# Performance work log

Measured on AMD Instinct MI355X. Metric: run time of the kernel, lower is better.

The kernel has to match this reference:

```python
import jax, jax.numpy as jnp
import numpy as np

EPS = 1e-13

def masked_softmax(scores, mask):
    # scores: [B, L1, L2], mask: [B, L2] binary float
    # ESIM-style: softmax(scores * mask) * mask, renormalized.
    m = mask[:, None, :]                      # [B, 1, L2]
    r = jax.nn.softmax(scores * m, axis=-1) * m
    return r / (r.sum(axis=-1, keepdims=True) + EPS)

def weighted_sum(attn, tensor, mask):
    # attn: [B, L1, L2], tensor: [B, L2, D], mask: [B, L1]
    return jnp.matmul(attn, tensor) * mask[:, :, None]

def setup_inputs() -> dict:
    key = jax.random.key(0)
    k1, k2, k3, k4 = jax.random.split(key, 4)
    B, Lp, Lh, D = 64, 512, 512, 600
    encoded_premise = jax.random.normal(k1, (B, Lp, D), dtype=jnp.float32)
    encoded_hypothesis = jax.random.normal(k2, (B, Lh, D), dtype=jnp.float32)
    # binary padding masks (1 = valid token)
    premise_mask = (jax.random.uniform(k3, (B, Lp)) > 0.15).astype(jnp.float32)
    hypothesis_mask = (jax.random.uniform(k4, (B, Lh)) > 0.15).astype(jnp.float32)
    return {"encoded_premise": encoded_premise, "premise_mask": premise_mask,
            "encoded_hypothesis": encoded_hypothesis, "hypothesis_mask": hypothesis_mask}

def reference(encoded_premise, premise_mask, encoded_hypothesis, hypothesis_mask):
    # shared cross-attention score matrix [B, Lp, Lh]
    attn = jnp.einsum('bpd,bhd->bph', encoded_premise, encoded_hypothesis)
    a_p = masked_softmax(attn, hypothesis_mask)                    # [B, Lp, Lh]
    a_h = masked_softmax(attn.transpose(0, 2, 1), premise_mask)    # [B, Lh, Lp]
    weighted_premise = weighted_sum(a_p, encoded_hypothesis, premise_mask)      # [B, Lp, D]
    weighted_hypothesis = weighted_sum(a_h, encoded_premise, hypothesis_mask)   # [B, Lh, D]
    return (weighted_premise, weighted_hypothesis)
```

## Files before the change

kernel.cpp:

```cpp
#include <hip/hip_runtime.h>
#include <hip/hip_bf16.h>

#define DEVB 64
#define LSEQ 512
#define DDIM 600

typedef short short8 __attribute__((ext_vector_type(8)));
typedef float f32x4 __attribute__((ext_vector_type(4)));
typedef _Float16 f16x8 __attribute__((ext_vector_type(8)));
typedef _Float16 f16x4 __attribute__((ext_vector_type(4)));

constexpr int LDP = 40;

__device__ __forceinline__ unsigned short f2bf(float x) {
    union { float f; unsigned u; } v; v.f = x;
    unsigned r = v.u + 0x7fffu + ((v.u >> 16) & 1u);
    return (unsigned short)(r >> 16);
}
__device__ __forceinline__ unsigned pk16(float a, float b) {
    union { _Float16 h[2]; unsigned u; } p;
    p.h[0] = (_Float16)a; p.h[1] = (_Float16)b;
    return p.u;
}
__device__ __forceinline__ f32x4 mfma16(short8 a, short8 b, f32x4 c) {
    return __builtin_amdgcn_mfma_f32_16x16x32_bf16(a, b, c, 0, 0, 0);
}
__device__ __forceinline__ f32x4 mfma16h(f16x8 a, f16x8 b, f32x4 c) {
    return __builtin_amdgcn_mfma_f32_16x16x32_f16(a, b, c, 0, 0, 0);
}

__global__ __launch_bounds__(256) void transcvt3(
    const float* __restrict__ P, const float* __restrict__ H,
    _Float16* __restrict__ pT, _Float16* __restrict__ hT)
{
    int blk = blockIdx.x;
    const float* X; _Float16* XT;
    const int half = DEVB * 40;
    if (blk < half) { X = P; XT = pT; }
    else { blk -= half; X = H; XT = hT; }

    int b   = blk / 40;
    int rem = blk % 40;
    int r0  = (rem / 5) << 6;
    int d0  = (rem % 5) << 7;
    const float* Xb = X + (size_t)b * LSEQ * DDIM;

    __shared__ unsigned T32[2][64 * 33];
    const int t  = threadIdx.x;
    const int rp = t >> 3;
    const int dc = (t & 7) << 3;

#pragma unroll
    for (int ht_ = 0; ht_ < 2; ++ht_) {
        int dd = d0 + (ht_ << 6) + dc;
        if (dd < DDIM) {
            const float* s0 = Xb + (size_t)(r0 + 2 * rp) * DDIM + dd;
            const float* s1 = s0 + DDIM;
            float4 a0 = *(const float4*)s0, a1 = *(const float4*)(s0 + 4);
            float4 b0 = *(const float4*)s1, b1 = *(const float4*)(s1 + 4);
            float xa[8] = {a0.x, a0.y, a0.z, a0.w, a1.x, a1.y, a1.z, a1.w};
            float xb[8] = {b0.x, b0.y, b0.z, b0.w, b1.x, b1.y, b1.z, b1.w};
#pragma unroll
            for (int j = 0; j < 8; ++j)
                T32[ht_][(dc + j) * 33 + rp] = pk16(xa[j], xb[j]);
        }
    }
    __syncthreads();

    const int dl = t >> 2;
    const int q  = t & 3;
#pragma unroll
    for (int ht_ = 0; ht_ < 2; ++ht_) {
        int d = d0 + (ht_ << 6) + dl;
        if (d < DDIM) {
            unsigned buf[8];
#pragma unroll
            for (int i = 0; i < 8; ++i)
                buf[i] = T32[ht_][dl * 33 + q * 8 + i];
            unsigned* dst = (unsigned*)(XT + ((size_t)b * DDIM + d) * LSEQ + r0) + q * 8;
            *(uint4*)(dst)     = *(uint4*)&buf[0];
            *(uint4*)(dst + 4) = *(uint4*)&buf[4];
        }
    }
}

__global__ __launch_bounds__(256) void attn_gemm(
    const float* __restrict__ P, const float* __restrict__ H,
    float* __restrict__ attn)
{
    const int bid = blockIdx.x;
    const int swz = (bid & 7) * 128 + (bid >> 3);
    const int b  = swz >> 4;
    const int pt = ((swz >> 2) & 3) << 7;
    const int ht = (swz & 3) << 7;
    const float* Pb = P + ((size_t)b * LSEQ + pt) * DDIM;
    const float* Hb = H + ((size_t)b * LSEQ + ht) * DDIM;
    float* Ab = attn + (size_t)b * LSEQ * LSEQ;

    __shared__ _Float16 Ah[2][128 * 32], Al[2][128 * 32], Bh[2][128 * 32];

    const int t    = threadIdx.x;
    const int lane = t & 63;
    const int wave = t >> 6;
    const int wm = (wave >> 1) << 6;
    const int wn = (wave & 1) << 6;
    const int fr = lane & 15;
    const int fq = lane >> 4;
    const int srow = t >> 2;
    const int sc8  = (t & 3) << 3;

    const int wchunk = (t & 3) ^ ((srow >> 1) & 3);
    const int woff   = srow * 32 + (wchunk << 3);
    const int rcoff  = ((fq ^ ((fr >> 1) & 3)) << 3);

    float4 pf[8];
    const float4 fz = {0.f, 0.f, 0.f, 0.f};
    auto issue = [&](int k0) {
        bool ok = (k0 + sc8) < DDIM;
#pragma unroll
        for (int r = 0; r < 2; ++r) {
            size_t base = (size_t)(srow + (r << 6)) * DDIM + k0 + sc8;
            if (ok) {
                pf[r * 4 + 0] = *(const float4*)(Pb + base);
                pf[r * 4 + 1] = *(const float4*)(Pb + base + 4);
                pf[r * 4 + 2] = *(const float4*)(Hb + base);
                pf[r * 4 + 3] = *(const float4*)(Hb + base + 4);
            } else {
                pf[r * 4 + 0] = fz; pf[r * 4 + 1] = fz;
                pf[r * 4 + 2] = fz; pf[r * 4 + 3] = fz;
            }
        }
    };
    auto wr = [&](int buf) {
#pragma unroll
        for (int r = 0; r < 2; ++r) {
            float4 a0 = pf[r * 4 + 0], a1 = pf[r * 4 + 1];
            float4 h0 = pf[r * 4 + 2], h1 = pf[r * 4 + 3];
            float af[8] = {a0.x, a0.y, a0.z, a0.w, a1.x, a1.y, a1.z, a1.w};
            float hf[8] = {h0.x, h0.y, h0.z, h0.w, h1.x, h1.y, h1.z, h1.w};
            f16x8 hi, lo, bh;
#pragma unroll
            for (int j = 0; j < 8; ++j) {
                hi[j] = (_Float16)af[j];
                lo[j] = (_Float16)(af[j] - (float)hi[j]);
                bh[j] = (_Float16)hf[j];
            }
            int off = woff + (r << 11);
            *(f16x8*)&Ah[buf][off] = hi;
            *(f16x8*)&Al[buf][off] = lo;
            *(f16x8*)&Bh[buf][off] = bh;
        }
    };

    issue(0);
    wr(0);
    issue(32);
    __syncthreads();

    f32x4 acc[4][4];
#pragma unroll
    for (int i = 0; i < 4; ++i)
#pragma unroll
        for (int j = 0; j < 4; ++j) acc[i][j] = (f32x4){0.f, 0.f, 0.f, 0.f};

    constexpr int NK = 19;
    int cur = 0;
    for (int it = 0; it < NK; ++it) {
        f16x8 ah[4], al[4], bh[4];
#pragma unroll
        for (int i = 0; i < 4; ++i) {
            int ra = (wm + (i << 4) + fr) * 32 + rcoff;
            int rb = (wn + (i << 4) + fr) * 32 + rcoff;
            ah[i] = *(const f16x8*)&Ah[cur][ra];
            al[i] = *(const f16x8*)&Al[cur][ra];
            bh[i] = *(const f16x8*)&Bh[cur][rb];
        }
        if (it + 1 < NK) {
            wr(cur ^ 1);
            if (it + 2 < NK) issue((it + 2) << 5);
        }
#pragma unroll
        for (int mi = 0; mi < 4; ++mi)
#pragma unroll
            for (int ni = 0; ni < 4; ++ni) {
                f32x4 c = acc[mi][ni];
                c = mfma16h(ah[mi], bh[ni], c);
                c = mfma16h(al[mi], bh[ni], c);
                acc[mi][ni] = c;
            }
        __syncthreads();
        cur ^= 1;
    }

#pragma unroll
    for (int mi = 0; mi < 4; ++mi)
#pragma unroll
        for (int ni = 0; ni < 4; ++ni)
#pragma unroll
            for (int j = 0; j < 4; ++j) {
                int p = pt + wm + (mi << 4) + (fq << 2) + j;
                int h = ht + wn + (ni << 4) + fr;
                Ab[(size_t)p * LSEQ + h] = acc[mi][ni][j];
            }
}

__global__ __launch_bounds__(256) void stats_w1(
    const float* __restrict__ attn, const float* __restrict__ hmask,
    const float* __restrict__ pmask,
    float* __restrict__ M1, float* __restrict__ R1,
    _Float16* __restrict__ W1,
    float* __restrict__ Mp, float* __restrict__ Tp, float* __restrict__ Sp)
{
    int b      = blockIdx.x >> 3;
    int stripe = blockIdx.x & 7;
    int lane   = threadIdx.x & 63;
    int wave   = threadIdx.x >> 6;
    const float* hm = hmask + (b << 9);
    const float* pm = pmask + (b << 9);

    float4 m0 = *(const float4*)(hm + (lane << 3));
    float4 m1 = *(const float4*)(hm + (lane << 3) + 4);
    float mk[8] = {m0.x, m0.y, m0.z, m0.w, m1.x, m1.y, m1.z, m1.w};

    float cM[8], cT[8], cS[8];
#pragma unroll
    for (int j = 0; j < 8; ++j) { cM[j] = -1e30f; cT[j] = 0.f; cS[j] = 0.f; }

    for (int i = 0; i < 16; ++i) {
        int row   = (stripe << 6) + (wave << 4) + i;
        int rowid = (b << 9) + row;
        const float* rp = attn + (size_t)rowid * LSEQ + (lane << 3);
        float4 s0 = *(const float4*)rp;
        float4 s1 = *(const float4*)(rp + 4);
        float s[8] = {s0.x, s0.y, s0.z, s0.w, s1.x, s1.y, s1.z, s1.w};

        float v[8];
#pragma unroll
        for (int j = 0; j < 8; ++j) v[j] = s[j] * mk[j];
        float mx = -1e30f;
#pragma unroll
        for (int j = 0; j < 8; ++j) mx = fmaxf(mx, v[j]);
#pragma unroll
        for (int off = 32; off; off >>= 1) mx = fmaxf(mx, __shfl_xor(mx, off));

        float e[8], T = 0.f, S = 0.f;
#pragma unroll
        for (int j = 0; j < 8; ++j) { e[j] = __expf(v[j] - mx); T += mk[j] * e[j]; S += e[j]; }
#pragma unroll
        for (int off = 32; off; off >>= 1) { T += __shfl_xor(T, off); S += __shfl_xor(S, off); }
        float R = 1.f / (T + 1e-13f * S);

        if (W1) {
            union { f16x8 v8; _Float16 h[8]; } wv;
#pragma unroll
            for (int j = 0; j < 8; ++j) wv.h[j] = (_Float16)(mk[j] * e[j] * R);
            *(f16x8*)(W1 + (size_t)rowid * LSEQ + (lane << 3)) = wv.v8;
        }
        if (lane == 0) { M1[rowid] = mx; R1[rowid] = R; }

        float pmv = pm[row];
#pragma unroll
        for (int j = 0; j < 8; ++j) {
            float v2 = s[j] * pmv;
            float nm = fmaxf(cM[j], v2);
            float sc = __expf(cM[j] - nm);
            float e2 = __expf(v2 - nm);
            cT[j] = cT[j] * sc + pmv * e2;
            cS[j] = cS[j] * sc + e2;
            cM[j] = nm;
        }
    }

    __shared__ float LM[4][512], LT[4][512], LS[4][512];
#pragma unroll
    for (int j = 0; j < 8; ++j) {
        int c = (lane << 3) + j;
        LM[wave][c] = cM[j]; LT[wave][c] = cT[j]; LS[wave][c] = cS[j];
    }
    __syncthreads();

    size_t base = (size_t)((b << 3) + stripe) * 512;
    for (int cc = threadIdx.x; cc < 512; cc += 256) {
        float gm = fmaxf(fmaxf(LM[0][cc], LM[1][cc]), fmaxf(LM[2][cc], LM[3][cc]));
        float gT = 0.f, gS = 0.f;
#pragma unroll
        for (int w = 0; w < 4; ++w) {
            float sc = __expf(LM[w][cc] - gm);
            gT += LT[w][cc] * sc;
            gS += LS[w][cc] * sc;
        }
        Mp[base + cc] = gm; Tp[base + cc] = gT; Sp[base + cc] = gS;
    }
}

__global__ __launch_bounds__(256) void col_merge(
    const float* __restrict__ Mp, const float* __restrict__ Tp,
    const float* __restrict__ Sp, float* __restrict__ M2, float* __restrict__ R2)
{
    int b = blockIdx.x >> 1;
    int c = ((blockIdx.x & 1) << 8) + threadIdx.x;
    float gm = -1e30f, gT = 0.f, gS = 0.f;
#pragma unroll
    for (int st = 0; st < 8; ++st) {
        size_t idx = (size_t)((b << 3) + st) * 512 + c;
        float m = Mp[idx], tt = Tp[idx], ss = Sp[idx];
        float nm  = fmaxf(gm, m);
        float sc1 = __expf(gm - nm), sc2 = __expf(m - nm);
        gT = gT * sc1 + tt * sc2;
        gS = gS * sc1 + ss * sc2;
        gm = nm;
    }
    M2[(b << 9) + c] = gm;
    R2[(b << 9) + c] = 1.f / (gT + 1e-13f * gS);
}

__global__ __launch_bounds__(256) void w2gen3(
    const float* __restrict__ attn, const float* __restrict__ pmask,
    const float* __restrict__ Mp, const float* __restrict__ Tp,
    const float* __restrict__ Sp, _Float16* __restrict__ W2)
{
    int blk = blockIdx.x;
    int b  = blk >> 5;
    int p0 = ((blk >> 2) & 7) << 6;
    int h0 = (blk & 3) << 7;
    const float* Ab = attn + (size_t)b * LSEQ * LSEQ;
    const float* pm = pmask + (b << 9);

    __shared__ float sM[128], sR[128];
    __shared__ unsigned T32[128 * 33];
    const int t = threadIdx.x;
    if (t < 128) {
        float gm = -1e30f, gT = 0.f, gS = 0.f;
#pragma unroll
        for (int st = 0; st < 8; ++st) {
            size_t idx = (size_t)((b << 3) + st) * 512 + h0 + t;
            float m = Mp[idx], tt = Tp[idx], ss = Sp[idx];
            float nm  = fmaxf(gm, m);
            float sc1 = __expf(gm - nm), sc2 = __expf(m - nm);
            gT = gT * sc1 + tt * sc2;
            gS = gS * sc1 + ss * sc2;
            gm = nm;
        }
        sM[t] = gm;
        sR[t] = 1.f / (gT + 1e-13f * gS);
    }
    __syncthreads();

#pragma unroll
    for (int it = 0; it < 4; ++it) {
        int g  = t + (it << 8);
        int pp = g >> 5;
        int hc = (g & 31) << 2;
        const float* s0 = Ab + (size_t)(p0 + 2 * pp) * LSEQ + h0 + hc;
        float4 xa = *(const float4*)s0;
        float4 xb = *(const float4*)(s0 + LSEQ);
        float pa = pm[p0 + 2 * pp];
        float pb = pm[p0 + 2 * pp + 1];
        float a[4] = {xa.x, xa.y, xa.z, xa.w};
        float bb[4] = {xb.x, xb.y, xb.z, xb.w};
#pragma unroll
        for (int j = 0; j < 4; ++j) {
            float wa = (pa != 0.f) ? __expf(a[j]  - sM[hc + j]) * sR[hc + j] : 0.f;
            float wb = (pb != 0.f) ? __expf(bb[j] - sM[hc + j]) * sR[hc + j] : 0.f;
            T32[(hc + j) * 33 + pp] = pk16(wa, wb);
        }
    }
    __syncthreads();

    const int hl = t >> 1;
    const int q  = t & 1;
    unsigned buf[16];
#pragma unroll
    for (int i = 0; i < 16; ++i)
        buf[i] = T32[hl * 33 + q * 16 + i];
    unsigned* dst = (unsigned*)(W2 + ((size_t)(b << 9) + h0 + hl) * LSEQ + p0) + q * 16;
#pragma unroll
    for (int i = 0; i < 4; ++i)
        *(uint4*)(dst + 4 * i) = *(uint4*)&buf[4 * i];
}

__global__ __launch_bounds__(256) void gemm_fp16(
    const _Float16* __restrict__ W, const _Float16* __restrict__ BT,
    const float* __restrict__ mask_m, float* __restrict__ out)
{
    const int bid = blockIdx.x;
    const int swz = (bid & 7) * 160 + (bid >> 3);
    const int b   = swz / 20;
    const int rem = swz % 20;
    const int m0  = (rem / 5) << 7;
    const int n0  = (rem % 5) << 7;
    const _Float16* Wb = W  + (size_t)b * LSEQ * LSEQ;
    const _Float16* Bb = BT + (size_t)b * DDIM * LSEQ;

    __shared__ _Float16 Wl[2][128 * 32];
    __shared__ _Float16 Bl[2][128 * 32];

    const int t    = threadIdx.x;
    const int lane = t & 63;
    const int wave = t >> 6;
    const int wm = (wave >> 1) << 6;
    const int wn = (wave & 1) << 6;
    const int fr = lane & 15;
    const int fq = lane >> 4;
    const int srow = t >> 2;
    const int sc8  = (t & 3) << 3;

    const int wchunk = (t & 3) ^ ((srow >> 1) & 3);
    const int woff   = srow * 32 + (wchunk << 3);
    const int rcoff  = ((fq ^ ((fr >> 1) & 3)) << 3);

    f16x8 pw[2], pb[2];
    const f16x8 zz = {0, 0, 0, 0, 0, 0, 0, 0};
    auto issue = [&](int k0) {
#pragma unroll
        for (int r = 0; r < 2; ++r) {
            int row = srow + (r << 6);
            pw[r] = *(const f16x8*)(Wb + (size_t)(m0 + row) * LSEQ + k0 + sc8);
            int nrow = n0 + row;
            pb[r] = (nrow < DDIM) ? *(const f16x8*)(Bb + (size_t)nrow * LSEQ + k0 + sc8) : zz;
        }
    };
    auto wr = [&](int buf) {
#pragma unroll
        for (int r = 0; r < 2; ++r) {
            int off = woff + (r << 11);
            *(f16x8*)&Wl[buf][off] = pw[r];
            *(f16x8*)&Bl[buf][off] = pb[r];
        }
    };

    issue(0);
    wr(0);
    issue(32);
    __syncthreads();

    f32x4 acc[4][4];
#pragma unroll
    for (int i = 0; i < 4; ++i)
#pragma unroll
        for (int j = 0; j < 4; ++j) acc[i][j] = (f32x4){0.f, 0.f, 0.f, 0.f};

    constexpr int NK = 16;
    int cur = 0;
    for (int it = 0; it < NK; ++it) {
        f16x8 af[4], bfr[4];
#pragma unroll
        for (int i = 0; i < 4; ++i) {
            af[i]  = *(const f16x8*)&Wl[cur][(wm + (i << 4) + fr) * 32 + rcoff];
            bfr[i] = *(const f16x8*)&Bl[cur][(wn + (i << 4) + fr) * 32 + rcoff];
        }
        if (it + 1 < NK) {
            wr(cur ^ 1);
            if (it + 2 < NK) issue((it + 2) << 5);
        }
#pragma unroll
        for (int mi = 0; mi < 4; ++mi)
#pragma unroll
            for (int ni = 0; ni < 4; ++ni)
                acc[mi][ni] = mfma16h(af[mi], bfr[ni], acc[mi][ni]);
        __syncthreads();
        cur ^= 1;
    }

    const float* mmb = mask_m + (b << 9) + m0;
#pragma unroll
    for (int mi = 0; mi < 4; ++mi)
#pragma unroll
        for (int j = 0; j < 4; ++j) {
            int row = wm + (mi << 4) + (fq << 2) + j;
            float mm = mmb[row];
#pragma unroll
            for (int ni = 0; ni < 4; ++ni) {
                int d = n0 + wn + (ni << 4) + fr;
                if (d < DDIM)
                    out[((size_t)(b << 9) + m0 + row) * DDIM + d] = mm * acc[mi][ni][j];
            }
        }
}

template <int TRANSA>
__global__ __launch_bounds__(256) void wsum(
    const float* __restrict__ attn, const float* __restrict__ Bsrc,
    const float* __restrict__ mask_k, const float* __restrict__ mask_m,
    const float* __restrict__ Mst, const float* __restrict__ Rst,
    float* __restrict__ out)
{
    const int blk = blockIdx.x;
    const int b   = blk / 20;
    const int rem = blk % 20;
    const int m0  = (rem / 5) << 7;
    const int n0  = (rem % 5) << 7;

    const float* Ab  = attn + (size_t)b * LSEQ * LSEQ;
    const float* Bb  = Bsrc + (size_t)b * LSEQ * DDIM;
    const float* mkb = mask_k + (b << 9);

    __shared__ unsigned short Wl[128 * LDP];
    __shared__ unsigned short Bl[128 * LDP];
    __shared__ float Ml[128], Rl[128], Mm[128];

    const int t    = threadIdx.x;
    const int lane = t & 63;
    const int wave = t >> 6;
    const int wm = (wave >> 1) << 6;
    const int wn = (wave & 1) << 6;
    const int fr = lane & 15;
    const int fq = lane >> 4;

    if (t < 128) {
        Ml[t] = Mst[(b << 9) + m0 + t];
        Rl[t] = Rst[(b << 9) + m0 + t];
        Mm[t] = mask_m[(b << 9) + m0 + t];
    }
    __syncthreads();

    f32x4 acc[4][4];
#pragma unroll
    for (int i = 0; i < 4; ++i)
#pragma unroll
        for (int j = 0; j < 4; ++j) acc[i][j] = (f32x4){0.f, 0.f, 0.f, 0.f};

    for (int k0 = 0; k0 < LSEQ; k0 += 32) {
        if constexpr (TRANSA == 0) {
#pragma unroll
            for (int r = 0; r < 4; ++r) {
                int idx = t + (r << 8);
                int row = idx >> 3;
                int c4  = (idx & 7) << 2;
                float4 x  = *(const float4*)(Ab + (size_t)(m0 + row) * LSEQ + k0 + c4);
                float4 km = *(const float4*)(mkb + k0 + c4);
                float Mv = Ml[row], Rv = Rl[row];
                ushort4 w;
                w.x = (km.x != 0.f) ? f2bf(__expf(x.x - Mv) * Rv) : (unsigned short)0;
                w.y = (km.y != 0.f) ? f2bf(__expf(x.y - Mv) * Rv) : (unsigned short)0;
                w.z = (km.z != 0.f) ? f2bf(__expf(x.z - Mv) * Rv) : (unsigned short)0;
                w.w = (km.w != 0.f) ? f2bf(__expf(x.w - Mv) * Rv) : (unsigned short)0;
                *(ushort4*)&Wl[row * LDP + c4] = w;
            }
        } else {
#pragma unroll
            for (int r = 0; r < 4; ++r) {
                int mh = t & 127;
                int pq = (t >> 7) + (r << 1);
                float Mv = Ml[mh], Rv = Rl[mh];
                ushort4 w;
#pragma unroll
                for (int j = 0; j < 4; ++j) {
                    int k = k0 + (pq << 2) + j;
                    float x  = Ab[(size_t)k * LSEQ + m0 + mh];
                    float km = mkb[k];
                    ((unsigned short*)&w)[j] =
                        (km != 0.f) ? f2bf(__expf(x - Mv) * Rv) : (unsigned short)0;
                }
                *(ushort4*)&Wl[mh * LDP + (pq << 2)] = w;
            }
        }
#pragma unroll
        for (int r = 0; r < 4; ++r) {
            int d  = t & 127;
            int kq = (t >> 7) + (r << 1);
            bool valid = (n0 + d) < DDIM;
            ushort4 v;
#pragma unroll
            for (int j = 0; j < 4; ++j) {
                int k = k0 + (kq << 2) + j;
                float x = valid ? Bb[(size_t)k * DDIM + n0 + d] : 0.f;
                ((unsigned short*)&v)[j] = f2bf(x);
            }
            *(ushort4*)&Bl[d * LDP + (kq << 2)] = v;
        }
        __syncthreads();

        short8 af[4], bfr[4];
#pragma unroll
        for (int i = 0; i < 4; ++i) {
            af[i]  = *(const short8*)&Wl[(wm + (i << 4) + fr) * LDP + (fq << 3)];
            bfr[i] = *(const short8*)&Bl[(wn + (i << 4) + fr) * LDP + (fq << 3)];
        }
#pragma unroll
        for (int mi = 0; mi < 4; ++mi)
#pragma unroll
            for (int ni = 0; ni < 4; ++ni)
                acc[mi][ni] = mfma16(af[mi], bfr[ni], acc[mi][ni]);
        __syncthreads();
    }

#pragma unroll
    for (int mi = 0; mi < 4; ++mi)
#pragma unroll
        for (int j = 0; j < 4; ++j) {
            int row = wm + (mi << 4) + (fq << 2) + j;
            float mm = Mm[row];
#pragma unroll
            for (int ni = 0; ni < 4; ++ni) {
                int d = n0 + wn + (ni << 4) + fr;
                if (d < DDIM)
                    out[((size_t)(b << 9) + m0 + row) * DDIM + d] = mm * acc[mi][ni][j];
            }
        }
}

extern "C" void kernel_launch(void* const* d_in, const int* in_sizes, int n_in,
                              void* d_out, int out_size, void* d_ws, size_t ws_size,
                              hipStream_t stream)
{
    const float* P  = (const float*)d_in[0];
    const float* pm = (const float*)d_in[1];
    const float* H  = (const float*)d_in[2];
    const float* hm = (const float*)d_in[3];
    float* out = (float*)d_out;
    char* o  = (char*)d_out;
    char* ws = (char*)d_ws;

    const size_t E = (size_t)DEVB * LSEQ * DDIM;

    _Float16* hT = (_Float16*)(o + 78643200);
    _Float16* W1 = (_Float16*)(o + 117964800);

    const size_t fast_need = 143654912;

    if (ws_size >= fast_need) {
        float*     attn = (float*)ws;
        _Float16*  pT   = (_Float16*)(ws + 67108864);
        _Float16*  W2   = (_Float16*)(ws + 67108864 + 39321600);
        float*     Mp   = (float*)(ws + 139984896);
        float*     Tp   = Mp + (size_t)DEVB * 8 * 512;
        float*     Sp   = Tp + (size_t)DEVB * 8 * 512;
        float*     M1   = Sp + (size_t)DEVB * 8 * 512;
        float*     R1   = M1 + DEVB * LSEQ;

        transcvt3<<<DEVB * 80, 256, 0, stream>>>(P, H, pT, hT);
        attn_gemm<<<DEVB * 16, 256, 0, stream>>>(P, H, attn);
        stats_w1<<<DEVB * 8, 256, 0, stream>>>(attn, hm, pm, M1, R1, W1, Mp, Tp, Sp);
        w2gen3<<<DEVB * 32, 256, 0, stream>>>(attn, pm, Mp, Tp, Sp, W2);
        gemm_fp16<<<DEVB * 20, 256, 0, stream>>>(W1, hT, pm, out);
        gemm_fp16<<<DEVB * 20, 256, 0, stream>>>(W2, pT, hm, out + E);
    } else {
        float* attn = (float*)ws;
        float* Mp   = (float*)(ws + 67108864);
        float* Tp   = Mp + (size_t)DEVB * 8 * 512;
        float* Sp   = Tp + (size_t)DEVB * 8 * 512;
        float* M1   = Sp + (size_t)DEVB * 8 * 512;
        float* R1   = M1 + DEVB * LSEQ;
        float* M2   = R1 + DEVB * LSEQ;
        float* R2   = M2 + DEVB * LSEQ;

        attn_gemm<<<DEVB * 16, 256, 0, stream>>>(P, H, attn);
        stats_w1<<<DEVB * 8, 256, 0, stream>>>(attn, hm, pm, M1, R1, nullptr, Mp, Tp, Sp);
        col_merge<<<DEVB * 2, 256, 0, stream>>>(Mp, Tp, Sp, M2, R2);
        wsum<0><<<DEVB * 20, 256, 0, stream>>>(attn, H, hm, pm, M1, R1, out);
        wsum<1><<<DEVB * 20, 256, 0, stream>>>(attn, P, pm, hm, M2, R2, out + E);
    }
}
```

Before: 321.4 us.

## Fuse transpose-convert into weighted-sum GEMM and merge both GEMMs into one launch

Result: no change. 315.1 us (-1.9%).

```diff
diff --git a/kernel.cpp b/kernel.cpp
--- a/kernel.cpp
+++ b/kernel.cpp
@@ -27,61 +27,6 @@
 }
 __device__ __forceinline__ f32x4 mfma16h(f16x8 a, f16x8 b, f32x4 c) {
     return __builtin_amdgcn_mfma_f32_16x16x32_f16(a, b, c, 0, 0, 0);
-}
-
-__global__ __launch_bounds__(256) void transcvt3(
-    const float* __restrict__ P, const float* __restrict__ H,
-    _Float16* __restrict__ pT, _Float16* __restrict__ hT)
-{
-    int blk = blockIdx.x;
-    const float* X; _Float16* XT;
-    const int half = DEVB * 40;
-    if (blk < half) { X = P; XT = pT; }
-    else { blk -= half; X = H; XT = hT; }
-
-    int b   = blk / 40;
-    int rem = blk % 40;
-    int r0  = (rem / 5) << 6;
-    int d0  = (rem % 5) << 7;
-    const float* Xb = X + (size_t)b * LSEQ * DDIM;
-
-    __shared__ unsigned T32[2][64 * 33];
-    const int t  = threadIdx.x;
-    const int rp = t >> 3;
-    const int dc = (t & 7) << 3;
-
-#pragma unroll
-    for (int ht_ = 0; ht_ < 2; ++ht_) {
-        int dd = d0 + (ht_ << 6) + dc;
-        if (dd < DDIM) {
-            const float* s0 = Xb + (size_t)(r0 + 2 * rp) * DDIM + dd;
-            const float* s1 = s0 + DDIM;
-            float4 a0 = *(const float4*)s0, a1 = *(const float4*)(s0 + 4);
-            float4 b0 = *(const float4*)s1, b1 = *(const float4*)(s1 + 4);
-            float xa[8] = {a0.x, a0.y, a0.z, a0.w, a1.x, a1.y, a1.z, a1.w};
-            float xb[8] = {b0.x, b0.y, b0.z, b0.w, b1.x, b1.y, b1.z, b1.w};
-#pragma unroll
-            for (int j = 0; j < 8; ++j)
-                T32[ht_][(dc + j) * 33 + rp] = pk16(xa[j], xb[j]);
-        }
-    }
-    __syncthreads();
-
-    const int dl = t >> 2;
-    const int q  = t & 3;
-#pragma unroll
-    for (int ht_ = 0; ht_ < 2; ++ht_) {
-        int d = d0 + (ht_ << 6) + dl;
-        if (d < DDIM) {
-            unsigned buf[8];
-#pragma unroll
-            for (int i = 0; i < 8; ++i)
-                buf[i] = T32[ht_][dl * 33 + q * 8 + i];
-            unsigned* dst = (unsigned*)(XT + ((size_t)b * DDIM + d) * LSEQ + r0) + q * 8;
-            *(uint4*)(dst)     = *(uint4*)&buf[0];
-            *(uint4*)(dst + 4) = *(uint4*)&buf[4];
-        }
-    }
 }
 
 __global__ __launch_bounds__(256) void attn_gemm(
@@ -379,21 +324,31 @@
         *(uint4*)(dst + 4 * i) = *(uint4*)&buf[4 * i];
 }
 
-__global__ __launch_bounds__(256) void gemm_fp16(
-    const _Float16* __restrict__ W, const _Float16* __restrict__ BT,
-    const float* __restrict__ mask_m, float* __restrict__ out)
+__global__ __launch_bounds__(256) void gemm_dual(
+    const _Float16* __restrict__ W1, const _Float16* __restrict__ W2,
+    const float* __restrict__ P, const float* __restrict__ H,
+    const float* __restrict__ pmask, const float* __restrict__ hmask,
+    float* __restrict__ out)
 {
-    const int bid = blockIdx.x;
+    int bid = blockIdx.x;
+    const _Float16* W; const float* Bsrc; const float* maskm; float* o;
+    if (bid < DEVB * 20) {
+        W = W1; Bsrc = H; maskm = pmask; o = out;
+    } else {
+        bid -= DEVB * 20;
+        W = W2; Bsrc = P; maskm = hmask;
+        o = out + (size_t)DEVB * LSEQ * DDIM;
+    }
     const int swz = (bid & 7) * 160 + (bid >> 3);
     const int b   = swz / 20;
     const int rem = swz % 20;
     const int m0  = (rem / 5) << 7;
     const int n0  = (rem % 5) << 7;
-    const _Float16* Wb = W  + (size_t)b * LSEQ * LSEQ;
-    const _Float16* Bb = BT + (size_t)b * DDIM * LSEQ;
+    const _Float16* Wb = W + (size_t)b * LSEQ * LSEQ;
+    const float*    Bb = Bsrc + (size_t)b * LSEQ * DDIM;
 
     __shared__ _Float16 Wl[2][128 * 32];
-    __shared__ _Float16 Bl[2][128 * 32];
+    __shared__ unsigned Bl[2][128 * 20];
 
     const int t    = threadIdx.x;
     const int lane = t & 63;
@@ -402,30 +357,47 @@
     const int wn = (wave & 1) << 6;
     const int fr = lane & 15;
     const int fq = lane >> 4;
+
     const int srow = t >> 2;
     const int sc8  = (t & 3) << 3;
-
     const int wchunk = (t & 3) ^ ((srow >> 1) & 3);
-    const int woff   = srow * 32 + (wchunk << 3);
+    const int woffA  = srow * 32 + (wchunk << 3);
     const int rcoff  = ((fq ^ ((fr >> 1) & 3)) << 3);
 
-    f16x8 pw[2], pb[2];
-    const f16x8 zz = {0, 0, 0, 0, 0, 0, 0, 0};
+    const int kp = t >> 4;
+    const int dg = t & 15;
+    const int dcol = n0 + (dg << 3);
+    const bool bok = dcol < DDIM;
+
+    f16x8 pw[2];
+    float4 pbv[4];
+    const float4 fz = {0.f, 0.f, 0.f, 0.f};
     auto issue = [&](int k0) {
-#pragma unroll
-        for (int r = 0; r < 2; ++r) {
-            int row = srow + (r << 6);
-            pw[r] = *(const f16x8*)(Wb + (size_t)(m0 + row) * LSEQ + k0 + sc8);
-            int nrow = n0 + row;
-            pb[r] = (nrow < DDIM) ? *(const f16x8*)(Bb + (size_t)nrow * LSEQ + k0 + sc8) : zz;
-        }
+        pw[0] = *(const f16x8*)(Wb + (size_t)(m0 + srow) * LSEQ + k0 + sc8);
+        pw[1] = *(const f16x8*)(Wb + (size_t)(m0 + srow + 64) * LSEQ + k0 + sc8);
+        if (bok) {
+            const float* r0 = Bb + (size_t)(k0 + 2 * kp) * DDIM + dcol;
+            const float* r1 = r0 + DDIM;
+            pbv[0] = *(const float4*)r0;
+            pbv[1] = *(const float4*)(r0 + 4);
+            pbv[2] = *(const float4*)r1;
+            pbv[3] = *(const float4*)(r1 + 4);
+        } else { pbv[0] = fz; pbv[1] = fz; pbv[2] = fz; pbv[3] = fz; }
     };
     auto wr = [&](int buf) {
-#pragma unroll
-        for (int r = 0; r < 2; ++r) {
-            int off = woff + (r << 11);
-            *(f16x8*)&Wl[buf][off] = pw[r];
-            *(f16x8*)&Bl[buf][off] = pb[r];
+        *(f16x8*)&Wl[buf][woffA]             = pw[0];
+        *(f16x8*)&Wl[buf][woffA + (64 * 32)] = pw[1];
+        float a[8] = {pbv[0].x, pbv[0].y, pbv[0].z, pbv[0].w,
+                      pbv[1].x, pbv[1].y, pbv[1].z, pbv[1].w};
+        float c[8] = {pbv[2].x, pbv[2].y, pbv[2].z, pbv[2].w,
+                      pbv[3].x, pbv[3].y, pbv[3].z, pbv[3].w};
+        unsigned w[8];
+#pragma unroll
+        for (int j = 0; j < 8; ++j) w[j] = pk16(a[j], c[j]);
+#pragma unroll
+        for (int jo = 0; jo < 8; ++jo) {
+            int jj = (jo + dg) & 7;
+            Bl[buf][((dg << 3) + jj) * 20 + kp] = w[jj];
         }
     };
 
@@ -446,8 +418,10 @@
         f16x8 af[4], bfr[4];
 #pragma unroll
         for (int i = 0; i < 4; ++i) {
-            af[i]  = *(const f16x8*)&Wl[cur][(wm + (i << 4) + fr) * 32 + rcoff];
-            bfr[i] = *(const f16x8*)&Bl[cur][(wn + (i << 4) + fr) * 32 + rcoff];
+            af[i] = *(const f16x8*)&Wl[cur][(wm + (i << 4) + fr) * 32 + rcoff];
+            union { uint4 u; f16x8 h; } bu;
+            bu.u = *(const uint4*)&Bl[cur][(wn + (i << 4) + fr) * 20 + (fq << 2)];
+            bfr[i] = bu.h;
         }
         if (it + 1 < NK) {
             wr(cur ^ 1);
@@ -462,7 +436,7 @@
         cur ^= 1;
     }
 
-    const float* mmb = mask_m + (b << 9) + m0;
+    const float* mmb = maskm + (b << 9) + m0;
 #pragma unroll
     for (int mi = 0; mi < 4; ++mi)
 #pragma unroll
@@ -473,7 +447,7 @@
             for (int ni = 0; ni < 4; ++ni) {
                 int d = n0 + wn + (ni << 4) + fr;
                 if (d < DDIM)
-                    out[((size_t)(b << 9) + m0 + row) * DDIM + d] = mm * acc[mi][ni][j];
+                    o[((size_t)(b << 9) + m0 + row) * DDIM + d] = mm * acc[mi][ni][j];
             }
         }
 }
@@ -609,32 +583,26 @@
     const float* H  = (const float*)d_in[2];
     const float* hm = (const float*)d_in[3];
     float* out = (float*)d_out;
-    char* o  = (char*)d_out;
     char* ws = (char*)d_ws;
 
     const size_t E = (size_t)DEVB * LSEQ * DDIM;
 
-    _Float16* hT = (_Float16*)(o + 78643200);
-    _Float16* W1 = (_Float16*)(o + 117964800);
-
-    const size_t fast_need = 143654912;
+    const size_t fast_need = 137625600;
 
     if (ws_size >= fast_need) {
         float*     attn = (float*)ws;
-        _Float16*  pT   = (_Float16*)(ws + 67108864);
-        _Float16*  W2   = (_Float16*)(ws + 67108864 + 39321600);
-        float*     Mp   = (float*)(ws + 139984896);
+        _Float16*  W1   = (_Float16*)(ws + 67108864);
+        _Float16*  W2   = (_Float16*)(ws + 67108864 + 33554432);
+        float*     Mp   = (float*)(ws + 134217728);
         float*     Tp   = Mp + (size_t)DEVB * 8 * 512;
         float*     Sp   = Tp + (size_t)DEVB * 8 * 512;
         float*     M1   = Sp + (size_t)DEVB * 8 * 512;
         float*     R1   = M1 + DEVB * LSEQ;
 
-        transcvt3<<<DEVB * 80, 256, 0, stream>>>(P, H, pT, hT);
         attn_gemm<<<DEVB * 16, 256, 0, stream>>>(P, H, attn);
         stats_w1<<<DEVB * 8, 256, 0, stream>>>(attn, hm, pm, M1, R1, W1, Mp, Tp, Sp);
         w2gen3<<<DEVB * 32, 256, 0, stream>>>(attn, pm, Mp, Tp, Sp, W2);
-        gemm_fp16<<<DEVB * 20, 256, 0, stream>>>(W1, hT, pm, out);
-        gemm_fp16<<<DEVB * 20, 256, 0, stream>>>(W2, pT, hm, out + E);
+        gemm_dual<<<DEVB * 40, 256, 0, stream>>>(W1, W2, P, H, pm, hm, out);
     } else {
         float* attn = (float*)ws;
         float* Mp   = (float*)(ws + 67108864);
```
